# Optimization experiments

Hardware: AMD Instinct MI355X
Metric: run time of the kernel (lower is better)

Reference implementation:

```python
import jax, jax.numpy as jnp
import numpy as np

B, S, D = 2, 2048, 768
H = 12
HD = D // H


def setup_inputs() -> dict:
    key = jax.random.key(0)
    ks = jax.random.split(key, 9)
    s_in = 1.0 / np.sqrt(D)
    return {
        "x": jax.random.normal(ks[0], (B, S, D), dtype=jnp.float32),
        "wq": jax.random.normal(ks[1], (D, D), dtype=jnp.float32) * s_in,
        "bq": jax.random.normal(ks[2], (D,), dtype=jnp.float32) * 0.01,
        "wk": jax.random.normal(ks[3], (D, D), dtype=jnp.float32) * s_in,
        "bk": jax.random.normal(ks[4], (D,), dtype=jnp.float32) * 0.01,
        "wv": jax.random.normal(ks[5], (D, D), dtype=jnp.float32) * s_in,
        "bv": jax.random.normal(ks[6], (D,), dtype=jnp.float32) * 0.01,
        "wo": jax.random.normal(ks[7], (D, D), dtype=jnp.float32) * s_in,
        "bo": jax.random.normal(ks[8], (D,), dtype=jnp.float32) * 0.01,
    }


def reference(x, wq, bq, wk, bk, wv, bv, wo, bo):
    b, s, _ = x.shape
    # projections -> [b, h, s, hd]
    def proj(w, bias):
        return (x @ w + bias).reshape(b, s, H, HD).transpose(0, 2, 1, 3)
    q = proj(wq, bq)
    k = proj(wk, bk)
    v = proj(wv, bv)
    scores = jnp.einsum("bhqd,bhkd->bhqk", q, k)
    causal = jnp.triu(jnp.ones((s, s), dtype=bool), k=1)
    scores = jnp.where(causal, -jnp.inf, scores)
    attn = jax.nn.softmax(scores / np.sqrt(HD), axis=-1)
    # dropout p=0.0 -> identity
    ctx = jnp.einsum("bhqk,bhkd->bhqd", attn, v)
    ctx = ctx.transpose(0, 2, 1, 3).reshape(b, s, D)
    return ctx @ wo + bo
```

## Files before the change

kernel.cpp:

```cpp
#include <hip/hip_runtime.h>
#include <math.h>

#define BB  2
#define SS  2048
#define DD  768
#define HH  12
#define HDD 64
#define BSR (BB * SS)
#define NQT (SS / 64)
#define NCH 80

typedef __attribute__((ext_vector_type(8))) short bf16x8;
typedef __attribute__((ext_vector_type(4))) float f32x4;
typedef __attribute__((ext_vector_type(4))) int  i32x4;

__device__ inline f32x4 mfma16(bf16x8 a, bf16x8 b, f32x4 c) {
    return __builtin_amdgcn_mfma_f32_16x16x32_bf16(a, b, c, 0, 0, 0);
}

__device__ inline unsigned short f2b(float f) {
    unsigned int u = __float_as_uint(f);
    u += 0x7FFFu + ((u >> 16) & 1u);
    return (unsigned short)(u >> 16);
}
__device__ inline float b2f(unsigned short u) {
    return __uint_as_float((unsigned int)u << 16);
}

__device__ inline unsigned int cvt_pk_bf16(float lo, float hi) {
    unsigned int r;
    asm("v_cvt_pk_bf16_f32 %0, %1, %2" : "=v"(r) : "v"(lo), "v"(hi));
    return r;
}

__device__ inline void async_copy16(void* lds, const void* g) {
    __builtin_amdgcn_global_load_lds(
        (const __attribute__((address_space(1))) unsigned int*)g,
        (__attribute__((address_space(3))) unsigned int*)lds, 16, 0, 0);
}

__global__ __launch_bounds__(256) void conv_wT_kernel(
    const float* __restrict__ w0, const float* __restrict__ w1,
    const float* __restrict__ w2, const float* __restrict__ w3,
    unsigned short* __restrict__ o0, unsigned short* __restrict__ o1,
    unsigned short* __restrict__ o2, unsigned short* __restrict__ o3)
{
    const float* w = (blockIdx.z == 0) ? w0 : (blockIdx.z == 1) ? w1
                   : (blockIdx.z == 2) ? w2 : w3;
    unsigned short* o = (blockIdx.z == 0) ? o0 : (blockIdx.z == 1) ? o1
                      : (blockIdx.z == 2) ? o2 : o3;
    const int n0 = blockIdx.x * 64;
    const int k0 = blockIdx.y * 64;
    const int tid = threadIdx.x;

    __shared__ unsigned short tile[64][72];

#pragma unroll
    for (int p = 0; p < 4; ++p) {
        int c  = p * 256 + tid;
        int kr = c >> 4;
        int nc = (c & 15) * 4;
        float4 v = *(const float4*)&w[(size_t)(k0 + kr) * DD + n0 + nc];
        tile[nc + 0][kr] = f2b(v.x);
        tile[nc + 1][kr] = f2b(v.y);
        tile[nc + 2][kr] = f2b(v.z);
        tile[nc + 3][kr] = f2b(v.w);
    }
    __syncthreads();
#pragma unroll
    for (int p = 0; p < 2; ++p) {
        int c  = p * 256 + tid;
        int nr = c >> 3;
        int kc = (c & 7) * 8;
        *(i32x4*)&o[(size_t)(n0 + nr) * DD + k0 + kc] = *(const i32x4*)&tile[nr][kc];
    }
}

__device__ inline void mainloop_64x128(
    const unsigned short* __restrict__ A, const unsigned short* __restrict__ Bt,
    unsigned short (*As)[64], unsigned short (*Bs)[64],
    f32x4 acc[2][4], int m0, int n0, int tid, int mh, int nh, int l16, int quad)
{
    const int swz = l16 & 7;
    for (int k0 = 0; k0 < DD; k0 += 64) {
        __syncthreads();
#pragma unroll
        for (int p = 0; p < 2; ++p) {
            int c  = p * 256 + tid;
            int r  = c >> 3;
            int ch = (c & 7) ^ (r & 7);
            async_copy16(&As[r][(c & 7) * 8], &A[(size_t)(m0 + r) * DD + k0 + ch * 8]);
        }
#pragma unroll
        for (int p = 0; p < 4; ++p) {
            int c  = p * 256 + tid;
            int r  = c >> 3;
            int ch = (c & 7) ^ (r & 7);
            async_copy16(&Bs[r][(c & 7) * 8], &Bt[(size_t)(n0 + r) * DD + k0 + ch * 8]);
        }
        __syncthreads();
        bf16x8 af0[2], af1[2], bf0[4], bf1[4];
#pragma unroll
        for (int mt = 0; mt < 2; ++mt) {
            int r = mh * 32 + mt * 16 + l16;
            af0[mt] = *(const bf16x8*)&As[r][((quad    ) ^ swz) * 8];
            af1[mt] = *(const bf16x8*)&As[r][((quad + 4) ^ swz) * 8];
        }
#pragma unroll
        for (int nt = 0; nt < 4; ++nt) {
            int r = nh * 64 + nt * 16 + l16;
            bf0[nt] = *(const bf16x8*)&Bs[r][((quad    ) ^ swz) * 8];
            bf1[nt] = *(const bf16x8*)&Bs[r][((quad + 4) ^ swz) * 8];
        }
#pragma unroll
        for (int mt = 0; mt < 2; ++mt)
#pragma unroll
            for (int nt = 0; nt < 4; ++nt) {
                acc[mt][nt] = mfma16(af0[mt], bf0[nt], acc[mt][nt]);
                acc[mt][nt] = mfma16(af1[mt], bf1[nt], acc[mt][nt]);
            }
    }
}

__global__ __launch_bounds__(256) void qkv_gemm_kernel(
    const float* __restrict__ x,
    const unsigned short* __restrict__ wqT, const unsigned short* __restrict__ wkT,
    const unsigned short* __restrict__ wvT,
    const float* __restrict__ bq, const float* __restrict__ bk,
    const float* __restrict__ bv,
    unsigned short* __restrict__ Qg, unsigned short* __restrict__ Kg,
    unsigned short* __restrict__ Vg)
{
    const int which = blockIdx.z;
    const unsigned short* Bt = (which == 0) ? wqT : (which == 1) ? wkT : wvT;
    const float* bias        = (which == 0) ? bq  : (which == 1) ? bk  : bv;
    unsigned short* out      = (which == 0) ? Qg  : (which == 1) ? Kg  : Vg;
    const float qs           = (which == 0) ? 0.18033688011112042f : 1.0f;

    const int m0 = blockIdx.x * 64;
    const int n0 = blockIdx.y * 128;
    const int tid  = threadIdx.x;
    const int w    = tid >> 6;
    const int lane = tid & 63;
    const int quad = lane >> 4;
    const int l16  = lane & 15;
    const int mh   = w & 1;
    const int nh   = w >> 1;
    const int swz  = l16 & 7;

    __shared__ unsigned short smem[12288];
    unsigned short (*As)[64]  = (unsigned short(*)[64])smem;
    unsigned short (*Bs)[64]  = (unsigned short(*)[64])(smem + 4096);
    unsigned short (*T)[136]  = (unsigned short(*)[136])smem;

    f32x4 zero = {0.f, 0.f, 0.f, 0.f};
    f32x4 acc[2][4];
#pragma unroll
    for (int i = 0; i < 2; ++i)
#pragma unroll
        for (int j = 0; j < 4; ++j) acc[i][j] = zero;

    for (int k0 = 0; k0 < DD; k0 += 64) {
        __syncthreads();
#pragma unroll
        for (int p = 0; p < 2; ++p) {
            int c  = p * 256 + tid;
            int r  = c >> 3;
            int j  = c & 7;
            int ch = j ^ (r & 7);
            const float* src = &x[(size_t)(m0 + r) * DD + k0 + ch * 8];
            float4 f0 = *(const float4*)src;
            float4 f1 = *(const float4*)(src + 4);
            i32x4 tv;
            tv[0] = (int)cvt_pk_bf16(f0.x, f0.y);
            tv[1] = (int)cvt_pk_bf16(f0.z, f0.w);
            tv[2] = (int)cvt_pk_bf16(f1.x, f1.y);
            tv[3] = (int)cvt_pk_bf16(f1.z, f1.w);
            *(i32x4*)&As[r][j * 8] = tv;
        }
#pragma unroll
        for (int p = 0; p < 4; ++p) {
            int c  = p * 256 + tid;
            int r  = c >> 3;
            int ch = (c & 7) ^ (r & 7);
            async_copy16(&Bs[r][(c & 7) * 8], &Bt[(size_t)(n0 + r) * DD + k0 + ch * 8]);
        }
        __syncthreads();
        bf16x8 af0[2], af1[2], bf0[4], bf1[4];
#pragma unroll
        for (int mt = 0; mt < 2; ++mt) {
            int r = mh * 32 + mt * 16 + l16;
            af0[mt] = *(const bf16x8*)&As[r][((quad    ) ^ swz) * 8];
            af1[mt] = *(const bf16x8*)&As[r][((quad + 4) ^ swz) * 8];
        }
#pragma unroll
        for (int nt = 0; nt < 4; ++nt) {
            int r = nh * 64 + nt * 16 + l16;
            bf0[nt] = *(const bf16x8*)&Bs[r][((quad    ) ^ swz) * 8];
            bf1[nt] = *(const bf16x8*)&Bs[r][((quad + 4) ^ swz) * 8];
        }
#pragma unroll
        for (int mt = 0; mt < 2; ++mt)
#pragma unroll
            for (int nt = 0; nt < 4; ++nt) {
                acc[mt][nt] = mfma16(af0[mt], bf0[nt], acc[mt][nt]);
                acc[mt][nt] = mfma16(af1[mt], bf1[nt], acc[mt][nt]);
            }
    }

    __syncthreads();

    if (which < 2) {
#pragma unroll
        for (int nt = 0; nt < 4; ++nt) {
            const int col = nh * 64 + nt * 16 + l16;
            const float bvv = bias[n0 + col];
#pragma unroll
            for (int mt = 0; mt < 2; ++mt)
#pragma unroll
                for (int r = 0; r < 4; ++r)
                    T[mh * 32 + mt * 16 + quad * 4 + r][col] =
                        f2b((acc[mt][nt][r] + bvv) * qs);
        }
        __syncthreads();
#pragma unroll
        for (int p2 = 0; p2 < 4; ++p2) {
            int c    = p2 * 256 + tid;
            int row  = c >> 4;
            int ck   = c & 15;
            int head = ck >> 3;
            int wi   = ck & 7;
            int sg   = m0 + row;
            int bi   = sg >> 11, si = sg & 2047;
            int hcol = (n0 >> 6) + head;
            *(i32x4*)&out[(((size_t)(bi * HH + hcol)) * SS + si) * HDD + wi * 8] =
                *(const i32x4*)&T[row][head * 64 + wi * 8];
        }
    } else {
        for (int pass = 0; pass < 2; ++pass) {
            if (pass) __syncthreads();
            if (nh == pass) {
#pragma unroll
                for (int nt = 0; nt < 4; ++nt) {
                    const float bvv = bias[n0 + pass * 64 + nt * 16 + l16];
#pragma unroll
                    for (int mt = 0; mt < 2; ++mt) {
                        uint2 pk;
                        pk.x = cvt_pk_bf16(acc[mt][nt][0] + bvv, acc[mt][nt][1] + bvv);
                        pk.y = cvt_pk_bf16(acc[mt][nt][2] + bvv, acc[mt][nt][3] + bvv);
                        *(uint2*)&T[nt * 16 + l16][mh * 32 + mt * 16 + quad * 4] = pk;
                    }
                }
            }
            __syncthreads();
            const int bi   = m0 >> 11;
            const int s0   = m0 & 2047;
            const int hcol = (n0 >> 6) + pass;
#pragma unroll
            for (int p2 = 0; p2 < 2; ++p2) {
                int c    = p2 * 256 + tid;
                int drow = c >> 3;
                int wi   = c & 7;
                *(i32x4*)&out[(((size_t)(bi * HH + hcol)) * HDD + drow) * SS + s0 + wi * 8] =
                    *(const i32x4*)&T[drow][wi * 8];
            }
        }
    }
}

__global__ __launch_bounds__(256) void out_gemm_kernel(
    const unsigned short* __restrict__ cb, const unsigned short* __restrict__ woT,
    const float* __restrict__ bo, float* __restrict__ out)
{
    const int m0 = blockIdx.x * 64;
    const int n0 = blockIdx.y * 128;
    const int tid  = threadIdx.x;
    const int w    = tid >> 6;
    const int lane = tid & 63;
    const int quad = lane >> 4;
    const int l16  = lane & 15;
    const int mh   = w & 1;
    const int nh   = w >> 1;

    __shared__ unsigned short As[64][64];
    __shared__ unsigned short Bs[128][64];

    f32x4 zero = {0.f, 0.f, 0.f, 0.f};
    f32x4 acc[2][4];
#pragma unroll
    for (int i = 0; i < 2; ++i)
#pragma unroll
        for (int j = 0; j < 4; ++j) acc[i][j] = zero;

    mainloop_64x128(cb, woT, As, Bs, acc, m0, n0, tid, mh, nh, l16, quad);

#pragma unroll
    for (int nt = 0; nt < 4; ++nt) {
        const int n = n0 + nh * 64 + nt * 16 + l16;
        const float bvv = bo[n];
#pragma unroll
        for (int mt = 0; mt < 2; ++mt) {
            const int mbase = m0 + mh * 32 + mt * 16 + quad * 4;
#pragma unroll
            for (int r = 0; r < 4; ++r)
                out[(size_t)(mbase + r) * DD + n] = acc[mt][nt][r] + bvv;
        }
    }
}

__global__ __launch_bounds__(256, 4) void attn_mfma_kernel(
    const unsigned short* __restrict__ Qg, const unsigned short* __restrict__ Kg,
    const unsigned short* __restrict__ Vg, unsigned short* __restrict__ Opart,
    float* __restrict__ Lb)
{
    const int c = (NCH - 1) - blockIdx.x;
    int qt, ck;
    if (c < 8)       { qt = c;                             ck = 0;     }
    else if (c < 24) { int t = c - 8;  qt = 8  + (t >> 1); ck = t & 1; }
    else if (c < 48) { int t = c - 24; qt = 16 + t / 3;    ck = t % 3; }
    else             { int t = c - 48; qt = 24 + (t >> 2); ck = t & 3; }
    const int lo = ck * 8;
    const int hi = min(lo + 8, qt + 1);

    const int h  = blockIdx.y;
    const int b  = blockIdx.z;
    const int tid  = threadIdx.x;
    const int w    = tid >> 6;
    const int lane = tid & 63;
    const int quad = lane >> 4;
    const int l16  = lane & 15;
    const int q0   = qt * 64;

    const size_t bh = (size_t)(b * HH + h);
    const unsigned short* qp = Qg + bh * SS * HDD;
    const unsigned short* kp = Kg + bh * SS * HDD;
    const unsigned short* vp = Vg + bh * HDD * SS;

    unsigned short* op = Opart + ((size_t)bh * NCH + c) * 64 * HDD;
    float* lp = Lb + ((size_t)bh * NCH + c) * 64;

    const int qlocal = w * 16 + l16;
    const int query  = q0 + qlocal;

    __shared__ unsigned short Ks[64][64];
    __shared__ unsigned short Vt[64][64];
    __shared__ unsigned short PsT[4][16][72];
    unsigned short* slab = &PsT[w][0][0];

    const bf16x8 qb0 = *(const bf16x8*)&qp[(size_t)query * HDD + quad * 8];
    const bf16x8 qb1 = *(const bf16x8*)&qp[(size_t)query * HDD + 32 + quad * 8];

    const int pr  = tid >> 3;
    const int po8 = tid & 7;
    const int fs  = l16 & 7;

    i32x4 kpre[2], vpre[2];
#pragma unroll
    for (int p = 0; p < 2; ++p) {
        int r  = pr + p * 32;
        int gc = (po8 ^ (r & 7)) * 8;
        kpre[p] = *(const i32x4*)&kp[(size_t)(lo * 64 + r) * HDD + gc];
        vpre[p] = *(const i32x4*)&vp[(size_t)r * SS + lo * 64 + gc];
    }

    f32x4 zero = {0.f, 0.f, 0.f, 0.f};
    f32x4 o_acc[4];
    float l_i = 0.f;
#pragma unroll
    for (int i = 0; i < 4; ++i) o_acc[i] = zero;

    for (int kt = lo; kt < hi; ++kt) {
        const int k0 = kt * 64;
        __syncthreads();
#pragma unroll
        for (int p = 0; p < 2; ++p) {
            int r = pr + p * 32;
            *(i32x4*)&Ks[r][po8 * 8] = kpre[p];
            *(i32x4*)&Vt[r][po8 * 8] = vpre[p];
        }
        __syncthreads();

        if (kt + 1 < hi) {
            const int kn = (kt + 1) * 64;
#pragma unroll
            for (int p = 0; p < 2; ++p) {
                int r  = pr + p * 32;
                int gc = (po8 ^ (r & 7)) * 8;
                kpre[p] = *(const i32x4*)&kp[(size_t)(kn + r) * HDD + gc];
                vpre[p] = *(const i32x4*)&vp[(size_t)r * SS + kn + gc];
            }
        }

        f32x4 s_acc[4];
#pragma unroll
        for (int t = 0; t < 4; ++t) {
            const int row = t * 16 + l16;
            bf16x8 klo = *(const bf16x8*)&Ks[row][((quad    ) ^ fs) * 8];
            bf16x8 khi = *(const bf16x8*)&Ks[row][((quad + 4) ^ fs) * 8];
            s_acc[t] = mfma16(klo, qb0, zero);
            s_acc[t] = mfma16(khi, qb1, s_acc[t]);
        }

        float ps[4][4];
#pragma unroll
        for (int t = 0; t < 4; ++t)
#pragma unroll
            for (int r = 0; r < 4; ++r) {
                const int key = k0 + t * 16 + quad * 4 + r;
                float pv = exp2f(s_acc[t][r]);
                if (kt == qt && key > query) pv = 0.f;
                ps[t][r] = pv;
                l_i += pv;
            }

#pragma unroll
        for (int t = 0; t < 4; ++t) {
            uint2 pk;
            pk.x = cvt_pk_bf16(ps[t][0], ps[t][1]);
            pk.y = cvt_pk_bf16(ps[t][2], ps[t][3]);
            *(uint2*)&slab[l16 * 72 + t * 16 + quad * 4] = pk;
        }
        bf16x8 pb0 = *(const bf16x8*)&slab[l16 * 72 + quad * 8];
        bf16x8 pb1 = *(const bf16x8*)&slab[l16 * 72 + 32 + quad * 8];

#pragma unroll
        for (int t2 = 0; t2 < 4; ++t2) {
            const int row = t2 * 16 + l16;
            bf16x8 vlo = *(const bf16x8*)&Vt[row][((quad    ) ^ fs) * 8];
            bf16x8 vhi = *(const bf16x8*)&Vt[row][((quad + 4) ^ fs) * 8];
            o_acc[t2] = mfma16(vlo, pb0, o_acc[t2]);
            o_acc[t2] = mfma16(vhi, pb1, o_acc[t2]);
        }
    }

    l_i += __shfl_xor(l_i, 16);
    l_i += __shfl_xor(l_i, 32);
    if (quad == 0) lp[qlocal] = l_i;
#pragma unroll
    for (int t2 = 0; t2 < 4; ++t2) {
        uint2 pk;
        pk.x = cvt_pk_bf16(o_acc[t2][0], o_acc[t2][1]);
        pk.y = cvt_pk_bf16(o_acc[t2][2], o_acc[t2][3]);
        *(uint2*)&slab[l16 * 72 + t2 * 16 + quad * 4] = pk;
    }
#pragma unroll
    for (int p2 = 0; p2 < 2; ++p2) {
        int cc  = p2 * 64 + lane;
        int row = cc >> 3, dc = cc & 7;
        *(i32x4*)&op[(size_t)(w * 16 + row) * HDD + dc * 8] =
            *(const i32x4*)&slab[row * 72 + dc * 8];
    }
}

__global__ __launch_bounds__(256) void merge_kernel(
    const unsigned short* __restrict__ Opart, const float* __restrict__ Lb,
    unsigned short* __restrict__ cb)
{
    const int qt  = blockIdx.x;
    const int bhn = blockIdx.y;
    const int b   = bhn / HH, h = bhn % HH;
    const int tid = threadIdx.x;
    const int row = tid >> 2;
    const int d0  = (tid & 3) * 16;
    const int q   = qt * 64 + row;

    const int nch = (qt < 8) ? 1 : (qt < 16) ? 2 : (qt < 24) ? 3 : 4;
    const int cb0 = (qt < 8) ? qt
                  : (qt < 16) ? (8  + (qt - 8)  * 2)
                  : (qt < 24) ? (24 + (qt - 16) * 3)
                  :             (48 + (qt - 24) * 4);

    float suml = 0.f;
    float accv[16];
#pragma unroll
    for (int i = 0; i < 16; ++i) accv[i] = 0.f;

    for (int ci = 0; ci < nch; ++ci) {
        const size_t base = (size_t)bhn * NCH + cb0 + ci;
        suml += Lb[base * 64 + row];
        const unsigned short* o = Opart + (base * 64 + row) * HDD + d0;
        i32x4 va = *(const i32x4*)&o[0];
        i32x4 vb = *(const i32x4*)&o[8];
#pragma unroll
        for (int wd = 0; wd < 4; ++wd) {
            unsigned int ua = (unsigned int)va[wd];
            accv[wd * 2 + 0] += __uint_as_float(ua << 16);
            accv[wd * 2 + 1] += __uint_as_float(ua & 0xffff0000u);
            unsigned int ub = (unsigned int)vb[wd];
            accv[8 + wd * 2 + 0] += __uint_as_float(ub << 16);
            accv[8 + wd * 2 + 1] += __uint_as_float(ub & 0xffff0000u);
        }
    }
    const float inv = 1.0f / suml;
    unsigned int res[8];
#pragma unroll
    for (int i = 0; i < 8; ++i)
        res[i] = cvt_pk_bf16(accv[2 * i] * inv, accv[2 * i + 1] * inv);
    unsigned short* dst = &cb[((size_t)(b * SS + q)) * DD + h * HDD + d0];
    *(i32x4*)&dst[0] = *(const i32x4*)&res[0];
    *(i32x4*)&dst[8] = *(const i32x4*)&res[4];
}

extern "C" void kernel_launch(void* const* d_in, const int* in_sizes, int n_in,
                              void* d_out, int out_size, void* d_ws, size_t ws_size,
                              hipStream_t stream)
{
    const float* x  = (const float*)d_in[0];
    const float* wq = (const float*)d_in[1];
    const float* bq = (const float*)d_in[2];
    const float* wk = (const float*)d_in[3];
    const float* bk = (const float*)d_in[4];
    const float* wv = (const float*)d_in[5];
    const float* bv = (const float*)d_in[6];
    const float* wo = (const float*)d_in[7];
    const float* bo = (const float*)d_in[8];
    float* out = (float*)d_out;

    char* p = (char*)d_ws;
    const size_t XB  = (size_t)BSR * DD * 2;
    const size_t WB  = (size_t)DD * DD * 2;
    const size_t OPB = (size_t)BB * HH * NCH * 64 * HDD * 2;
    const size_t LBB = (size_t)BB * HH * NCH * 64 * 4;
    unsigned short* wqT = (unsigned short*)p;            p += WB;
    unsigned short* wkT = (unsigned short*)p;            p += WB;
    unsigned short* wvT = (unsigned short*)p;            p += WB;
    unsigned short* woT = (unsigned short*)p;            p += WB;
    unsigned short* Qg  = (unsigned short*)p;            p += XB;
    unsigned short* Kg  = (unsigned short*)p;            p += XB;
    unsigned short* Vg  = (unsigned short*)p;            p += XB;
    unsigned short* cb  = (unsigned short*)p;            p += XB;
    unsigned short* Opart = (unsigned short*)p;          p += OPB;
    float* Lb = (float*)p;                               p += LBB;

    conv_wT_kernel<<<dim3(DD / 64, DD / 64, 4), 256, 0, stream>>>(
        wq, wk, wv, wo, wqT, wkT, wvT, woT);
    qkv_gemm_kernel<<<dim3(BSR / 64, DD / 128, 3), 256, 0, stream>>>(
        x, wqT, wkT, wvT, bq, bk, bv, Qg, Kg, Vg);
    attn_mfma_kernel<<<dim3(NCH, HH, BB), 256, 0, stream>>>(
        Qg, Kg, Vg, Opart, Lb);
    merge_kernel<<<dim3(NQT, BB * HH), 256, 0, stream>>>(Opart, Lb, cb);
    out_gemm_kernel<<<dim3(BSR / 64, DD / 128), 256, 0, stream>>>(cb, woT, bo, out);
}
```

Baseline: 168.0 us.

## Double-buffer LDS tiles in QKV and output projection GEMMs

Both projection GEMMs now use two LDS buffers for the A and B tiles. The next K-tile's global loads (fp32 x converted to bf16, or async copies of weights) are issued before the MFMAs on the current tile, leaving one barrier per iteration instead of two. The aim is to hide global-load latency behind matrix math. In exchange, shared memory per block doubles to 48KB, which may cut occupancy, and more registers are held for prefetched data. The shared mainloop helper is inlined into each kernel.

New measurement: 161.2 us. -4.1%, faster.

```diff
diff --git a/kernel.cpp b/kernel.cpp
--- a/kernel.cpp
+++ b/kernel.cpp
@@ -9,6 +9,7 @@
 #define BSR (BB * SS)
 #define NQT (SS / 64)
 #define NCH 80
+#define NKT 12
 
 typedef __attribute__((ext_vector_type(8))) short bf16x8;
 typedef __attribute__((ext_vector_type(4))) float f32x4;
@@ -73,52 +74,6 @@
         int nr = c >> 3;
         int kc = (c & 7) * 8;
         *(i32x4*)&o[(size_t)(n0 + nr) * DD + k0 + kc] = *(const i32x4*)&tile[nr][kc];
-    }
-}
-
-__device__ inline void mainloop_64x128(
-    const unsigned short* __restrict__ A, const unsigned short* __restrict__ Bt,
-    unsigned short (*As)[64], unsigned short (*Bs)[64],
-    f32x4 acc[2][4], int m0, int n0, int tid, int mh, int nh, int l16, int quad)
-{
-    const int swz = l16 & 7;
-    for (int k0 = 0; k0 < DD; k0 += 64) {
-        __syncthreads();
-#pragma unroll
-        for (int p = 0; p < 2; ++p) {
-            int c  = p * 256 + tid;
-            int r  = c >> 3;
-            int ch = (c & 7) ^ (r & 7);
-            async_copy16(&As[r][(c & 7) * 8], &A[(size_t)(m0 + r) * DD + k0 + ch * 8]);
-        }
-#pragma unroll
-        for (int p = 0; p < 4; ++p) {
-            int c  = p * 256 + tid;
-            int r  = c >> 3;
-            int ch = (c & 7) ^ (r & 7);
-            async_copy16(&Bs[r][(c & 7) * 8], &Bt[(size_t)(n0 + r) * DD + k0 + ch * 8]);
-        }
-        __syncthreads();
-        bf16x8 af0[2], af1[2], bf0[4], bf1[4];
-#pragma unroll
-        for (int mt = 0; mt < 2; ++mt) {
-            int r = mh * 32 + mt * 16 + l16;
-            af0[mt] = *(const bf16x8*)&As[r][((quad    ) ^ swz) * 8];
-            af1[mt] = *(const bf16x8*)&As[r][((quad + 4) ^ swz) * 8];
-        }
-#pragma unroll
-        for (int nt = 0; nt < 4; ++nt) {
-            int r = nh * 64 + nt * 16 + l16;
-            bf0[nt] = *(const bf16x8*)&Bs[r][((quad    ) ^ swz) * 8];
-            bf1[nt] = *(const bf16x8*)&Bs[r][((quad + 4) ^ swz) * 8];
-        }
-#pragma unroll
-        for (int mt = 0; mt < 2; ++mt)
-#pragma unroll
-            for (int nt = 0; nt < 4; ++nt) {
-                acc[mt][nt] = mfma16(af0[mt], bf0[nt], acc[mt][nt]);
-                acc[mt][nt] = mfma16(af1[mt], bf1[nt], acc[mt][nt]);
-            }
     }
 }
 
@@ -148,10 +103,31 @@
     const int nh   = w >> 1;
     const int swz  = l16 & 7;
 
-    __shared__ unsigned short smem[12288];
-    unsigned short (*As)[64]  = (unsigned short(*)[64])smem;
-    unsigned short (*Bs)[64]  = (unsigned short(*)[64])(smem + 4096);
+    __shared__ unsigned short smem[24576];
+    unsigned short (*As0)[64] = (unsigned short(*)[64])smem;
+    unsigned short (*Bs0)[64] = (unsigned short(*)[64])(smem + 4096);
+    unsigned short (*As1)[64] = (unsigned short(*)[64])(smem + 12288);
+    unsigned short (*Bs1)[64] = (unsigned short(*)[64])(smem + 16384);
     unsigned short (*T)[136]  = (unsigned short(*)[136])smem;
+
+    const int rA0 = tid >> 3,          jA0 = tid & 7,          chA0 = jA0 ^ (rA0 & 7);
+    const int rA1 = (256 + tid) >> 3,  jA1 = tid & 7,          chA1 = jA1 ^ (rA1 & 7);
+    const float* xr0 = &x[(size_t)(m0 + rA0) * DD + chA0 * 8];
+    const float* xr1 = &x[(size_t)(m0 + rA1) * DD + chA1 * 8];
+    int ldsA0 = rA0 * 64 + jA0 * 8;
+    int ldsA1 = rA1 * 64 + jA1 * 8;
+
+    const unsigned short* gB[4];
+    int ldsB[4];
+#pragma unroll
+    for (int p = 0; p < 4; ++p) {
+        int c  = p * 256 + tid;
+        int r  = c >> 3;
+        int j  = c & 7;
+        int ch = j ^ (r & 7);
+        gB[p]   = &Bt[(size_t)(n0 + r) * DD + ch * 8];
+        ldsB[p] = r * 64 + j * 8;
+    }
 
     f32x4 zero = {0.f, 0.f, 0.f, 0.f};
     f32x4 acc[2][4];
@@ -160,32 +136,49 @@
 #pragma unroll
         for (int j = 0; j < 4; ++j) acc[i][j] = zero;
 
-    for (int k0 = 0; k0 < DD; k0 += 64) {
-        __syncthreads();
-#pragma unroll
-        for (int p = 0; p < 2; ++p) {
-            int c  = p * 256 + tid;
-            int r  = c >> 3;
-            int j  = c & 7;
-            int ch = j ^ (r & 7);
-            const float* src = &x[(size_t)(m0 + r) * DD + k0 + ch * 8];
-            float4 f0 = *(const float4*)src;
-            float4 f1 = *(const float4*)(src + 4);
-            i32x4 tv;
-            tv[0] = (int)cvt_pk_bf16(f0.x, f0.y);
-            tv[1] = (int)cvt_pk_bf16(f0.z, f0.w);
-            tv[2] = (int)cvt_pk_bf16(f1.x, f1.y);
-            tv[3] = (int)cvt_pk_bf16(f1.z, f1.w);
-            *(i32x4*)&As[r][j * 8] = tv;
-        }
-#pragma unroll
-        for (int p = 0; p < 4; ++p) {
-            int c  = p * 256 + tid;
-            int r  = c >> 3;
-            int ch = (c & 7) ^ (r & 7);
-            async_copy16(&Bs[r][(c & 7) * 8], &Bt[(size_t)(n0 + r) * DD + k0 + ch * 8]);
-        }
-        __syncthreads();
+    {
+        float4 pf0 = *(const float4*)(xr0);
+        float4 pf1 = *(const float4*)(xr0 + 4);
+        float4 pf2 = *(const float4*)(xr1);
+        float4 pf3 = *(const float4*)(xr1 + 4);
+#pragma unroll
+        for (int p = 0; p < 4; ++p)
+            async_copy16((unsigned short*)Bs0 + ldsB[p], gB[p]);
+        i32x4 tv;
+        tv[0] = (int)cvt_pk_bf16(pf0.x, pf0.y);
+        tv[1] = (int)cvt_pk_bf16(pf0.z, pf0.w);
+        tv[2] = (int)cvt_pk_bf16(pf1.x, pf1.y);
+        tv[3] = (int)cvt_pk_bf16(pf1.z, pf1.w);
+        *(i32x4*)((unsigned short*)As0 + ldsA0) = tv;
+        tv[0] = (int)cvt_pk_bf16(pf2.x, pf2.y);
+        tv[1] = (int)cvt_pk_bf16(pf2.z, pf2.w);
+        tv[2] = (int)cvt_pk_bf16(pf3.x, pf3.y);
+        tv[3] = (int)cvt_pk_bf16(pf3.z, pf3.w);
+        *(i32x4*)((unsigned short*)As1 + 0) = tv;
+        *(i32x4*)((unsigned short*)As0 + ldsA1) = tv;
+    }
+    __syncthreads();
+
+#pragma unroll
+    for (int t = 0; t < NKT; ++t) {
+        const int kn = (t + 1) * 64;
+        unsigned short (*As)[64] = (t & 1) ? As1 : As0;
+        unsigned short (*Bs)[64] = (t & 1) ? Bs1 : Bs0;
+        unsigned short (*An)[64] = (t & 1) ? As0 : As1;
+        unsigned short (*Bn)[64] = (t & 1) ? Bs0 : Bs1;
+        const bool more = (t + 1 < NKT);
+
+        float4 pf0, pf1, pf2, pf3;
+        if (more) {
+            pf0 = *(const float4*)(xr0 + kn);
+            pf1 = *(const float4*)(xr0 + kn + 4);
+            pf2 = *(const float4*)(xr1 + kn);
+            pf3 = *(const float4*)(xr1 + kn + 4);
+#pragma unroll
+            for (int p = 0; p < 4; ++p)
+                async_copy16((unsigned short*)Bn + ldsB[p], gB[p] + kn);
+        }
+
         bf16x8 af0[2], af1[2], bf0[4], bf1[4];
 #pragma unroll
         for (int mt = 0; mt < 2; ++mt) {
@@ -206,9 +199,22 @@
                 acc[mt][nt] = mfma16(af0[mt], bf0[nt], acc[mt][nt]);
                 acc[mt][nt] = mfma16(af1[mt], bf1[nt], acc[mt][nt]);
             }
-    }
-
-    __syncthreads();
+
+        if (more) {
+            i32x4 tv;
+            tv[0] = (int)cvt_pk_bf16(pf0.x, pf0.y);
+            tv[1] = (int)cvt_pk_bf16(pf0.z, pf0.w);
+            tv[2] = (int)cvt_pk_bf16(pf1.x, pf1.y);
+            tv[3] = (int)cvt_pk_bf16(pf1.z, pf1.w);
+            *(i32x4*)((unsigned short*)An + ldsA0) = tv;
+            tv[0] = (int)cvt_pk_bf16(pf2.x, pf2.y);
+            tv[1] = (int)cvt_pk_bf16(pf2.z, pf2.w);
+            tv[2] = (int)cvt_pk_bf16(pf3.x, pf3.y);
+            tv[3] = (int)cvt_pk_bf16(pf3.z, pf3.w);
+            *(i32x4*)((unsigned short*)An + ldsA1) = tv;
+        }
+        __syncthreads();
+    }
 
     if (which < 2) {
 #pragma unroll
@@ -281,9 +287,36 @@
     const int l16  = lane & 15;
     const int mh   = w & 1;
     const int nh   = w >> 1;
-
-    __shared__ unsigned short As[64][64];
-    __shared__ unsigned short Bs[128][64];
+    const int swz  = l16 & 7;
+
+    __shared__ unsigned short smem[24576];
+    unsigned short (*As0)[64] = (unsigned short(*)[64])smem;
+    unsigned short (*Bs0)[64] = (unsigned short(*)[64])(smem + 4096);
+    unsigned short (*As1)[64] = (unsigned short(*)[64])(smem + 12288);
+    unsigned short (*Bs1)[64] = (unsigned short(*)[64])(smem + 16384);
+
+    const unsigned short* gA[2];
+    int ldsA[2];
+#pragma unroll
+    for (int p = 0; p < 2; ++p) {
+        int c  = p * 256 + tid;
+        int r  = c >> 3;
+        int j  = c & 7;
+        int ch = j ^ (r & 7);
+        gA[p]   = &cb[(size_t)(m0 + r) * DD + ch * 8];
+        ldsA[p] = r * 64 + j * 8;
+    }
+    const unsigned short* gB[4];
+    int ldsB[4];
+#pragma unroll
+    for (int p = 0; p < 4; ++p) {
+        int c  = p * 256 + tid;
+        int r  = c >> 3;
+        int j  = c & 7;
+        int ch = j ^ (r & 7);
+        gB[p]   = &woT[(size_t)(n0 + r) * DD + ch * 8];
+        ldsB[p] = r * 64 + j * 8;
+    }
 
     f32x4 zero = {0.f, 0.f, 0.f, 0.f};
     f32x4 acc[2][4];
@@ -292,7 +325,49 @@
 #pragma unroll
         for (int j = 0; j < 4; ++j) acc[i][j] = zero;
 
-    mainloop_64x128(cb, woT, As, Bs, acc, m0, n0, tid, mh, nh, l16, quad);
+#pragma unroll
+    for (int p = 0; p < 2; ++p) async_copy16((unsigned short*)As0 + ldsA[p], gA[p]);
+#pragma unroll
+    for (int p = 0; p < 4; ++p) async_copy16((unsigned short*)Bs0 + ldsB[p], gB[p]);
+    __syncthreads();
+
+#pragma unroll
+    for (int t = 0; t < NKT; ++t) {
+        const int kn = (t + 1) * 64;
+        unsigned short (*As)[64] = (t & 1) ? As1 : As0;
+        unsigned short (*Bs)[64] = (t & 1) ? Bs1 : Bs0;
+        unsigned short (*An)[64] = (t & 1) ? As0 : As1;
+        unsigned short (*Bn)[64] = (t & 1) ? Bs0 : Bs1;
+        if (t + 1 < NKT) {
+#pragma unroll
+            for (int p = 0; p < 2; ++p)
+                async_copy16((unsigned short*)An + ldsA[p], gA[p] + kn);
+#pragma unroll
+            for (int p = 0; p < 4; ++p)
+                async_copy16((unsigned short*)Bn + ldsB[p], gB[p] + kn);
+        }
+        bf16x8 af0[2], af1[2], bf0[4], bf1[4];
+#pragma unroll
+        for (int mt = 0; mt < 2; ++mt) {
+            int r = mh * 32 + mt * 16 + l16;
+            af0[mt] = *(const bf16x8*)&As[r][((quad    ) ^ swz) * 8];
+            af1[mt] = *(const bf16x8*)&As[r][((quad + 4) ^ swz) * 8];
+        }
+#pragma unroll
+        for (int nt = 0; nt < 4; ++nt) {
+            int r = nh * 64 + nt * 16 + l16;
+            bf0[nt] = *(const bf16x8*)&Bs[r][((quad    ) ^ swz) * 8];
+            bf1[nt] = *(const bf16x8*)&Bs[r][((quad + 4) ^ swz) * 8];
+        }
+#pragma unroll
+        for (int mt = 0; mt < 2; ++mt)
+#pragma unroll
+            for (int nt = 0; nt < 4; ++nt) {
+                acc[mt][nt] = mfma16(af0[mt], bf0[nt], acc[mt][nt]);
+                acc[mt][nt] = mfma16(af1[mt], bf1[nt], acc[mt][nt]);
+            }
+        __syncthreads();
+    }
 
 #pragma unroll
     for (int nt = 0; nt < 4; ++nt) {
```
